# Performance work log

Hardware: AMD Instinct MI355X
Metric: run time of the kernel (lower is better)

The kernel has to match this reference:

```python
import jax, jax.numpy as jnp
import numpy as np

D_MODEL = 1024
N_HEAD = 16
D_K = 64
D_V = 64
D_INNER = 4096
MAX_REL = 16
EPS = 1e-6


def _rel_index(length_q, length_k):
    # Shaw-style clipped relative distance matrix -> indices into embedding table
    dist = jnp.arange(length_k)[None, :] - jnp.arange(length_q)[:, None]
    return jnp.clip(dist, -MAX_REL, MAX_REL) + MAX_REL  # [Lq, Lk] in [0, 2*MAX_REL]


def _layer_norm(x, gamma, beta):
    mu = jnp.mean(x, axis=-1, keepdims=True)
    var = jnp.var(x, axis=-1, keepdims=True)
    return (x - mu) / jnp.sqrt(var + EPS) * gamma + beta


def setup_inputs() -> dict:
    key = jax.random.key(0)
    ks = jax.random.split(key, 16)
    B, L = 8, 1024
    s = 0.02
    inp = {
        "q": jax.random.normal(ks[0], (B, L, D_MODEL), jnp.float32),
        "k": jax.random.normal(ks[1], (B, L, D_MODEL), jnp.float32),
        "v": jax.random.normal(ks[2], (B, L, D_MODEL), jnp.float32),
        "wq": jax.random.normal(ks[3], (D_MODEL, D_MODEL), jnp.float32) * s,
        "bq": jnp.zeros((D_MODEL,), jnp.float32),
        "wk": jax.random.normal(ks[4], (D_MODEL, D_MODEL), jnp.float32) * s,
        "bk": jnp.zeros((D_MODEL,), jnp.float32),
        "wv": jax.random.normal(ks[5], (D_MODEL, D_MODEL), jnp.float32) * s,
        "bv": jnp.zeros((D_MODEL,), jnp.float32),
        "wfc": jax.random.normal(ks[6], (D_MODEL, D_MODEL), jnp.float32) * s,
        "bfc": jnp.zeros((D_MODEL,), jnp.float32),
        "w1": jax.random.normal(ks[7], (D_MODEL, D_INNER), jnp.float32) * s,
        "b1": jnp.zeros((D_INNER,), jnp.float32),
        "w2": jax.random.normal(ks[8], (D_INNER, D_MODEL), jnp.float32) * s,
        "b2": jnp.zeros((D_MODEL,), jnp.float32),
        "ln_g": jnp.ones((D_MODEL,), jnp.float32),
        "ln_b": jnp.zeros((D_MODEL,), jnp.float32),
        "rel_k": jax.random.normal(ks[9], (2 * MAX_REL + 1, D_K), jnp.float32) * s,
        "rel_v": jax.random.normal(ks[10], (2 * MAX_REL + 1, D_V), jnp.float32) * s,
    }
    return inp


def reference(q, k, v, wq, bq, wk, bk, wv, bv, wfc, bfc, w1, b1, w2, b2, ln_g, ln_b, rel_k, rel_v):
    B, Lq, _ = q.shape
    Lk = k.shape[1]
    residual = q

    Q = q @ wq + bq  # [B, Lq, D]
    K = k @ wk + bk
    V = v @ wv + bv

    Qh = Q.reshape(B, Lq, N_HEAD, D_K)  # [B, Lq, H, dk]
    Kh = K.reshape(B, Lk, N_HEAD, D_K)
    Vh = V.reshape(B, Lk, N_HEAD, D_V)

    # content-content scores
    attn1 = jnp.einsum("bqhd,bkhd->bhqk", Qh, Kh)
    # content-position scores (Shaw relative position)
    idx = _rel_index(Lq, Lk)  # [Lq, Lk]
    k2 = rel_k[idx]           # [Lq, Lk, dk]
    attn2 = jnp.einsum("bqhd,qkd->bhqk", Qh, k2)

    attn = (attn1 + attn2) / jnp.sqrt(jnp.float32(D_K))
    attn = jax.nn.softmax(attn, axis=-1)  # dropout = identity (eval)

    weight1 = jnp.einsum("bhqk,bkhd->bhqd", attn, Vh)
    v2 = rel_v[idx]  # [Lq, Lk, dv]
    weight2 = jnp.einsum("bhqk,qkd->bhqd", attn, v2)

    out = (weight1 + weight2).transpose(0, 2, 1, 3).reshape(B, Lq, N_HEAD * D_V)
    out = out @ wfc + bfc
    out = out + residual
    out = _layer_norm(out, ln_g, ln_b)

    residual = out
    out2 = jax.nn.relu(out @ w1 + b1) @ w2 + b2
    out = _layer_norm(out2 + residual, ln_g, ln_b)  # same LN params reused, as in source
    return out
```

## Files before the change

kernel.cpp:

```cpp
#include <hip/hip_runtime.h>
#include <stdint.h>


typedef __bf16 bf16x8 __attribute__((ext_vector_type(8)));
typedef float  f32x4  __attribute__((ext_vector_type(4)));

__device__ __forceinline__ unsigned short f2bf(float f) {
  __bf16 h = (__bf16)f;
  union { __bf16 h; unsigned short u; } x; x.h = h;
  return x.u;
}
__device__ __forceinline__ float bf2f(unsigned short h) {
  union { unsigned u; float f; } x; x.u = ((unsigned)h) << 16; return x.f;
}

__device__ __forceinline__ void gload_lds16(
    const unsigned short* g,
    __attribute__((address_space(3))) unsigned int* l) {
  __builtin_amdgcn_global_load_lds(
      (const __attribute__((address_space(1))) unsigned int*)g, l, 16, 0, 0);
}

template<int EPI>
__global__ __launch_bounds__(256) void gemm_bt(
    const unsigned short* __restrict__ A,
    const unsigned short* __restrict__ Bt,
    const float* __restrict__ bias,
    void* __restrict__ Cout,
    int M, int N, int K)
{
  __shared__ __align__(16) unsigned short As[128 * 32];
  __shared__ __align__(16) unsigned short Bs[128 * 32];
  const int tid = threadIdx.x;
  const int lane = tid & 63, wv = tid >> 6;
  const int lq = lane >> 4, lm = lane & 15;
  const int wr = wv >> 1, wc = wv & 1;

  const int nx = gridDim.x;
  const int nwg = nx * gridDim.y;
  int bid = blockIdx.y * nx + blockIdx.x;
  bid = (bid & 7) * (nwg >> 3) + (bid >> 3);
  const int m0 = (bid / nx) * 128, n0 = (bid % nx) * 128;

  const unsigned short* ga0 = A  + (size_t)(m0 + (tid >> 2)) * K + (tid & 3) * 8;
  const unsigned short* gb0 = Bt + (size_t)(n0 + (tid >> 2)) * K + (tid & 3) * 8;
  const size_t rstep = (size_t)64 * K;

  __attribute__((address_space(3))) unsigned int* lA =
      (__attribute__((address_space(3))) unsigned int*)As + wv * 256;
  __attribute__((address_space(3))) unsigned int* lB =
      (__attribute__((address_space(3))) unsigned int*)Bs + wv * 256;

  const char* fa = (const char*)As + (wr * 64 + lm) * 64 + lq * 16;
  const char* fb = (const char*)Bs + (wc * 64 + lm) * 64 + lq * 16;

  f32x4 acc[4][4] = {};
  const int nk = K >> 5;
  for (int kt = 0; kt < nk; ++kt) {
    __syncthreads();
    gload_lds16(ga0,         lA);
    gload_lds16(ga0 + rstep, lA + 1024);
    gload_lds16(gb0,         lB);
    gload_lds16(gb0 + rstep, lB + 1024);
    ga0 += 32; gb0 += 32;
    __syncthreads();
    bf16x8 af[4], bfr[4];
    #pragma unroll
    for (int i = 0; i < 4; ++i) af[i]  = *(const bf16x8*)(fa + i * 16 * 64);
    #pragma unroll
    for (int j = 0; j < 4; ++j) bfr[j] = *(const bf16x8*)(fb + j * 16 * 64);
    #pragma unroll
    for (int i = 0; i < 4; ++i)
      #pragma unroll
      for (int j = 0; j < 4; ++j)
        acc[i][j] = __builtin_amdgcn_mfma_f32_16x16x32_bf16(af[i], bfr[j], acc[i][j], 0, 0, 0);
  }
  #pragma unroll
  for (int i = 0; i < 4; ++i) {
    #pragma unroll
    for (int j = 0; j < 4; ++j) {
      const int col = n0 + wc * 64 + j * 16 + lm;
      const float bv = bias[col];
      #pragma unroll
      for (int r = 0; r < 4; ++r) {
        const int row = m0 + wr * 64 + i * 16 + lq * 4 + r;
        float v = acc[i][j][r] + bv;
        if (EPI == 2) v = fmaxf(v, 0.0f);
        if (EPI == 1) ((float*)Cout)[(size_t)row * N + col] = v;
        else ((unsigned short*)Cout)[(size_t)row * N + col] = f2bf(v);
      }
    }
  }
}

__global__ __launch_bounds__(256) void tcast(
    const float* __restrict__ in, unsigned short* __restrict__ out, int R, int C)
{
  __shared__ float tile[32][33];
  const int tx = threadIdx.x & 31, ty = threadIdx.x >> 5;
  const int r0 = blockIdx.y * 32, c0 = blockIdx.x * 32;
  #pragma unroll
  for (int s = 0; s < 4; ++s)
    tile[ty + s * 8][tx] = in[(size_t)(r0 + ty + s * 8) * C + c0 + tx];
  __syncthreads();
  #pragma unroll
  for (int s = 0; s < 4; ++s)
    out[(size_t)(c0 + ty + s * 8) * R + r0 + tx] = f2bf(tile[tx][ty + s * 8]);
}

__global__ __launch_bounds__(256) void cast4(
    const float* __restrict__ in, unsigned short* __restrict__ out, int n)
{
  int i = (blockIdx.x * 256 + threadIdx.x) * 4;
  if (i < n) {
    float4 v = *(const float4*)(in + i);
    ushort4 o;
    o.x = f2bf(v.x); o.y = f2bf(v.y); o.z = f2bf(v.z); o.w = f2bf(v.w);
    *(ushort4*)(out + i) = o;
  }
}

__global__ __launch_bounds__(256) void vtrans(
    const unsigned short* __restrict__ VP, unsigned short* __restrict__ VPT)
{
  __shared__ unsigned short tile[64 * 66];
  const int pt = blockIdx.x, h = blockIdx.y, b = blockIdx.z;
  const int tid = threadIdx.x;
  const int p = tid >> 2, c0 = (tid & 3) * 16;
  const unsigned short* src = VP + (size_t)(b * 1024 + pt * 64 + p) * 1024 + h * 64 + c0;
  union { uint4 q; unsigned int u[4]; } t0, t1;
  t0.q = *(const uint4*)src;
  t1.q = *(const uint4*)(src + 8);
  #pragma unroll
  for (int e = 0; e < 4; ++e) {
    *(unsigned int*)&tile[p * 66 + c0 + e * 2]     = t0.u[e];
    *(unsigned int*)&tile[p * 66 + c0 + 8 + e * 2] = t1.u[e];
  }
  __syncthreads();
  const int d = tid >> 2, p0 = (tid & 3) * 16;
  union { uint4 q[2]; unsigned short s[16]; } ob;
  #pragma unroll
  for (int e = 0; e < 16; ++e) ob.s[e] = tile[(p0 + e) * 66 + d];
  unsigned short* dst = VPT + ((size_t)(h * 64 + d) * 8 + b) * 1024 + pt * 64 + p0;
  *(uint4*)dst       = ob.q[0];
  *(uint4*)(dst + 8) = ob.q[1];
}

__global__ __launch_bounds__(256, 3) void attn_flash(
    const unsigned short* __restrict__ Qp,
    const unsigned short* __restrict__ Kp,
    const unsigned short* __restrict__ VPT,
    const float* __restrict__ relk,
    const float* __restrict__ relv,
    unsigned short* __restrict__ ctx)
{
  const int qt = blockIdx.x, h = blockIdx.y, b = blockIdx.z;
  const int tid = threadIdx.x;
  const int lane = tid & 63, wv = tid >> 6;
  const int lq = lane >> 4, lm = lane & 15;

  __shared__ __align__(16) unsigned short Kt[64][72];
  __shared__ __align__(16) unsigned short Vt[64][72];
  __shared__ __align__(16) unsigned short Pt[64][72];
  __shared__ __align__(16) unsigned short relvT[64][32];
  __shared__ float qrel_s[64][33];
  __shared__ float Racc[64][33];

  const float CE = 0.125f * 1.44269504088896340736f;

  const int tok0 = b * 1024 + qt * 64;

  for (int i = tid; i < 64 * 33; i += 256) {
    const int rr = i / 33, ss = i - rr * 33;
    Racc[rr][ss] = 0.0f;
  }
  for (int i = tid; i < 64 * 32; i += 256) {
    const int dd = i >> 5, ss = i & 31;
    relvT[dd][ss] = f2bf(relv[ss * 64 + dd]);
  }

  bf16x8 qf0, qf1;
  {
    const unsigned short* qg = Qp + (size_t)(tok0 + wv * 16 + lm) * 1024 + h * 64;
    qf0 = *(const bf16x8*)(qg + lq * 8);
    qf1 = *(const bf16x8*)(qg + 32 + lq * 8);
  }

  #pragma unroll
  for (int t = 0; t < 3; ++t) {
    const int bin = t * 16 + lm;
    union { bf16x8 v; unsigned short s[8]; } rk0, rk1;
    #pragma unroll
    for (int e = 0; e < 8; ++e) { rk0.s[e] = 0; rk1.s[e] = 0; }
    if (bin < 33) {
      const float* rp = relk + bin * 64 + lq * 8;
      #pragma unroll
      for (int e = 0; e < 8; ++e) {
        rk0.s[e] = f2bf(rp[e]);
        rk1.s[e] = f2bf(rp[32 + e]);
      }
    }
    f32x4 Sr = {};
    Sr = __builtin_amdgcn_mfma_f32_16x16x32_bf16(qf0, rk0.v, Sr, 0, 0, 0);
    Sr = __builtin_amdgcn_mfma_f32_16x16x32_bf16(qf1, rk1.v, Sr, 0, 0, 0);
    if (bin < 33) {
      #pragma unroll
      for (int r = 0; r < 4; ++r) qrel_s[wv * 16 + lq * 4 + r][bin] = Sr[r] * CE;
    }
  }
  __syncthreads();

  float q0a[4], q32a[4];
  #pragma unroll
  for (int r = 0; r < 4; ++r) {
    const int rowl = wv * 16 + lq * 4 + r;
    q0a[r]  = qrel_s[rowl][0];
    q32a[r] = qrel_s[rowl][32];
  }

  union { bf16x8 v; unsigned short s[8]; } one8;
  #pragma unroll
  for (int e = 0; e < 8; ++e) one8.s[e] = 0x3F80;

  f32x4 Oa[4] = {};
  f32x4 Rs = {};
  float r0a[4] = {0, 0, 0, 0}, r32a[4] = {0, 0, 0, 0};

  const int srow = tid >> 2, scol = (tid & 3) * 16;
  const unsigned short* kg = Kp + (size_t)(b * 1024 + srow) * 1024 + h * 64 + scol;
  const unsigned short* vg = VPT + ((size_t)(h * 64 + srow) * 8 + b) * 1024 + scol;
  const int qa0 = qt * 64 + wv * 16;

  for (int kt = 0; kt < 16; ++kt) {
    __syncthreads();
    *(uint4*)&Kt[srow][scol]     = *(const uint4*)(kg);
    *(uint4*)&Kt[srow][scol + 8] = *(const uint4*)(kg + 8);
    *(uint4*)&Vt[srow][scol]     = *(const uint4*)(vg);
    *(uint4*)&Vt[srow][scol + 8] = *(const uint4*)(vg + 8);
    kg += 64 * 1024;
    vg += 64;
    __syncthreads();

    #pragma unroll
    for (int tj = 0; tj < 4; ++tj) {
      bf16x8 kf0 = *(const bf16x8*)(&Kt[tj * 16 + lm][lq * 8]);
      bf16x8 kf1 = *(const bf16x8*)(&Kt[tj * 16 + lm][32 + lq * 8]);
      f32x4 S = {};
      S = __builtin_amdgcn_mfma_f32_16x16x32_bf16(qf0, kf0, S, 0, 0, 0);
      S = __builtin_amdgcn_mfma_f32_16x16x32_bf16(qf1, kf1, S, 0, 0, 0);
      const int c0 = kt * 64 + tj * 16;
      if (c0 + 31 <= qa0) {
        #pragma unroll
        for (int r = 0; r < 4; ++r) {
          const float p = __builtin_amdgcn_exp2f(fmaf(S[r], CE, q0a[r]));
          r0a[r] += p;
          Pt[wv * 16 + lq * 4 + r][tj * 16 + lm] = f2bf(p);
        }
      } else if (c0 >= qa0 + 31) {
        #pragma unroll
        for (int r = 0; r < 4; ++r) {
          const float p = __builtin_amdgcn_exp2f(fmaf(S[r], CE, q32a[r]));
          r32a[r] += p;
          Pt[wv * 16 + lq * 4 + r][tj * 16 + lm] = f2bf(p);
        }
      } else {
        const int kpos = c0 + lm;
        #pragma unroll
        for (int r = 0; r < 4; ++r) {
          const int rowl = wv * 16 + lq * 4 + r;
          const int dist = kpos - (qt * 64 + rowl);
          const int bin = (dist < -16 ? 0 : (dist > 16 ? 32 : dist + 16));
          const float p = __builtin_amdgcn_exp2f(fmaf(S[r], CE, qrel_s[rowl][bin]));
          if (bin == 0)       r0a[r]  += p;
          else if (bin == 32) r32a[r] += p;
          else Racc[rowl][bin] = p;
          Pt[rowl][tj * 16 + lm] = f2bf(p);
        }
      }
    }
    __syncthreads();
    const int prow = wv * 16 + lm;
    bf16x8 pf0 = *(const bf16x8*)(&Pt[prow][lq * 8]);
    bf16x8 pf1 = *(const bf16x8*)(&Pt[prow][32 + lq * 8]);
    Rs = __builtin_amdgcn_mfma_f32_16x16x32_bf16(pf0, one8.v, Rs, 0, 0, 0);
    Rs = __builtin_amdgcn_mfma_f32_16x16x32_bf16(pf1, one8.v, Rs, 0, 0, 0);
    #pragma unroll
    for (int dt = 0; dt < 4; ++dt) {
      bf16x8 vf0 = *(const bf16x8*)(&Vt[dt * 16 + lm][lq * 8]);
      bf16x8 vf1 = *(const bf16x8*)(&Vt[dt * 16 + lm][32 + lq * 8]);
      Oa[dt] = __builtin_amdgcn_mfma_f32_16x16x32_bf16(pf0, vf0, Oa[dt], 0, 0, 0);
      Oa[dt] = __builtin_amdgcn_mfma_f32_16x16x32_bf16(pf1, vf1, Oa[dt], 0, 0, 0);
    }
  }

  #pragma unroll
  for (int r = 0; r < 4; ++r) {
    #pragma unroll
    for (int off = 1; off < 16; off <<= 1) {
      r0a[r]  += __shfl_xor(r0a[r],  off, 64);
      r32a[r] += __shfl_xor(r32a[r], off, 64);
    }
  }
  if (lm == 0) {
    #pragma unroll
    for (int r = 0; r < 4; ++r) Racc[wv * 16 + lq * 4 + r][0] = r0a[r];
  }
  __syncthreads();
  for (int i = tid; i < 64 * 32; i += 256) {
    const int rr = i >> 5, cc = i & 31;
    Pt[rr][cc] = f2bf(Racc[rr][cc]);
  }
  __syncthreads();

  bf16x8 raf = *(const bf16x8*)(&Pt[wv * 16 + lm][lq * 8]);
  #pragma unroll
  for (int dt = 0; dt < 4; ++dt) {
    bf16x8 rvb = *(const bf16x8*)(&relvT[dt * 16 + lm][lq * 8]);
    f32x4 O2 = {};
    O2 = __builtin_amdgcn_mfma_f32_16x16x32_bf16(raf, rvb, O2, 0, 0, 0);
    const float rv32 = relv[32 * 64 + dt * 16 + lm];
    #pragma unroll
    for (int r = 0; r < 4; ++r) {
      const int rowl = wv * 16 + lq * 4 + r;
      const float v = (Oa[dt][r] + O2[r] + r32a[r] * rv32) / Rs[r];
      ctx[(size_t)(tok0 + rowl) * 1024 + h * 64 + dt * 16 + lm] = f2bf(v);
    }
  }
}

template<bool WB>
__global__ __launch_bounds__(256) void ln_res(
    const float* __restrict__ x, const float* __restrict__ res,
    const float* __restrict__ g, const float* __restrict__ bta,
    float* __restrict__ of, unsigned short* __restrict__ ob)
{
  const int row = blockIdx.x;
  const int tid = threadIdx.x;
  __shared__ float red[8];
  const size_t base = (size_t)row * 1024 + tid * 4;
  const float4 xv = *(const float4*)(x + base);
  const float4 rv = *(const float4*)(res + base);
  float v0 = xv.x + rv.x, v1 = xv.y + rv.y, v2 = xv.z + rv.z, v3 = xv.w + rv.w;
  float s1 = v0 + v1 + v2 + v3;
  float s2 = v0 * v0 + v1 * v1 + v2 * v2 + v3 * v3;
  #pragma unroll
  for (int off = 1; off < 64; off <<= 1) {
    s1 += __shfl_xor(s1, off, 64);
    s2 += __shfl_xor(s2, off, 64);
  }
  const int wv = tid >> 6;
  if ((tid & 63) == 0) { red[wv * 2] = s1; red[wv * 2 + 1] = s2; }
  __syncthreads();
  s1 = red[0] + red[2] + red[4] + red[6];
  s2 = red[1] + red[3] + red[5] + red[7];
  const float mean = s1 * (1.f / 1024.f);
  const float var = s2 * (1.f / 1024.f) - mean * mean;
  const float rstd = rsqrtf(var + 1e-6f);
  const float4 gv = *(const float4*)(g + tid * 4);
  const float4 bv = *(const float4*)(bta + tid * 4);
  float y0 = (v0 - mean) * rstd * gv.x + bv.x;
  float y1 = (v1 - mean) * rstd * gv.y + bv.y;
  float y2 = (v2 - mean) * rstd * gv.z + bv.z;
  float y3 = (v3 - mean) * rstd * gv.w + bv.w;
  float4 yo; yo.x = y0; yo.y = y1; yo.z = y2; yo.w = y3;
  *(float4*)(of + base) = yo;
  if (WB) {
    ushort4 o;
    o.x = f2bf(y0); o.y = f2bf(y1); o.z = f2bf(y2); o.w = f2bf(y3);
    *(ushort4*)(ob + base) = o;
  }
}

extern "C" void kernel_launch(void* const* d_in, const int* in_sizes, int n_in,
                              void* d_out, int out_size, void* d_ws, size_t ws_size,
                              hipStream_t stream) {
  (void)in_sizes; (void)n_in; (void)out_size; (void)ws_size;
  const float* q    = (const float*)d_in[0];
  const float* k    = (const float*)d_in[1];
  const float* v    = (const float*)d_in[2];
  const float* wq   = (const float*)d_in[3];
  const float* bq   = (const float*)d_in[4];
  const float* wk   = (const float*)d_in[5];
  const float* bk   = (const float*)d_in[6];
  const float* wv_  = (const float*)d_in[7];
  const float* bv   = (const float*)d_in[8];
  const float* wfc  = (const float*)d_in[9];
  const float* bfc  = (const float*)d_in[10];
  const float* w1   = (const float*)d_in[11];
  const float* b1   = (const float*)d_in[12];
  const float* w2   = (const float*)d_in[13];
  const float* b2   = (const float*)d_in[14];
  const float* ln_g = (const float*)d_in[15];
  const float* ln_b = (const float*)d_in[16];
  const float* rel_k = (const float*)d_in[17];
  const float* rel_v = (const float*)d_in[18];

  char* ws = (char*)d_ws;
  const size_t MB = 1ull << 20;
  unsigned short* WQT  = (unsigned short*)(ws + 0 * MB);
  unsigned short* WKT  = (unsigned short*)(ws + 2 * MB);
  unsigned short* WVT  = (unsigned short*)(ws + 4 * MB);
  unsigned short* WFCT = (unsigned short*)(ws + 6 * MB);
  unsigned short* W1T  = (unsigned short*)(ws + 8 * MB);
  unsigned short* W2T  = (unsigned short*)(ws + 16 * MB);
  unsigned short* QP   = (unsigned short*)(ws + 24 * MB);
  unsigned short* KP   = (unsigned short*)(ws + 40 * MB);
  unsigned short* VP   = (unsigned short*)(ws + 56 * MB);
  unsigned short* QBF  = (unsigned short*)(ws + 72 * MB);
  unsigned short* KBF  = (unsigned short*)(ws + 88 * MB);
  unsigned short* VBF  = (unsigned short*)(ws + 104 * MB);
  unsigned short* VPT  = QBF;
  unsigned short* CTX  = KBF;
  float*          OTMP = (float*)(ws + 104 * MB);
  float*          X1F  = (float*)(ws + 24 * MB);
  unsigned short* X1BF = VP;
  unsigned short* HBUF = (unsigned short*)(ws + 72 * MB);
  float*          Y2   = (float*)(ws + 136 * MB);

  const dim3 blk(256);
  const int NTOK = 8192;

  tcast<<<dim3(32, 32), blk, 0, stream>>>(wq, WQT, 1024, 1024);
  tcast<<<dim3(32, 32), blk, 0, stream>>>(wk, WKT, 1024, 1024);
  tcast<<<dim3(32, 32), blk, 0, stream>>>(wv_, WVT, 1024, 1024);
  tcast<<<dim3(32, 32), blk, 0, stream>>>(wfc, WFCT, 1024, 1024);
  tcast<<<dim3(128, 32), blk, 0, stream>>>(w1, W1T, 1024, 4096);
  tcast<<<dim3(32, 128), blk, 0, stream>>>(w2, W2T, 4096, 1024);
  cast4<<<8192, blk, 0, stream>>>(q, QBF, NTOK * 1024);
  cast4<<<8192, blk, 0, stream>>>(k, KBF, NTOK * 1024);
  cast4<<<8192, blk, 0, stream>>>(v, VBF, NTOK * 1024);

  gemm_bt<0><<<dim3(8, 64), blk, 0, stream>>>(QBF, WQT, bq, QP, NTOK, 1024, 1024);
  gemm_bt<0><<<dim3(8, 64), blk, 0, stream>>>(KBF, WKT, bk, KP, NTOK, 1024, 1024);
  gemm_bt<0><<<dim3(8, 64), blk, 0, stream>>>(VBF, WVT, bv, VP, NTOK, 1024, 1024);

  vtrans<<<dim3(16, 16, 8), blk, 0, stream>>>(VP, VPT);

  attn_flash<<<dim3(16, 16, 8), blk, 0, stream>>>(QP, KP, VPT, rel_k, rel_v, CTX);

  gemm_bt<1><<<dim3(8, 64), blk, 0, stream>>>(CTX, WFCT, bfc, OTMP, NTOK, 1024, 1024);
  ln_res<true><<<8192, blk, 0, stream>>>(OTMP, q, ln_g, ln_b, X1F, X1BF);
  gemm_bt<2><<<dim3(32, 64), blk, 0, stream>>>(X1BF, W1T, b1, HBUF, NTOK, 4096, 1024);
  gemm_bt<1><<<dim3(8, 64), blk, 0, stream>>>(HBUF, W2T, b2, Y2, NTOK, 1024, 4096);
  ln_res<false><<<8192, blk, 0, stream>>>(Y2, X1F, ln_g, ln_b, (float*)d_out, nullptr);
}
```

Before: 659.8 us.

## Prefetch K/V tiles into registers, swizzle block order, remap P-tile row layout

```diff
diff --git a/kernel.cpp b/kernel.cpp
--- a/kernel.cpp
+++ b/kernel.cpp
@@ -154,7 +154,10 @@
     const float* __restrict__ relv,
     unsigned short* __restrict__ ctx)
 {
-  const int qt = blockIdx.x, h = blockIdx.y, b = blockIdx.z;
+  int id = (blockIdx.z * gridDim.y + blockIdx.y) * gridDim.x + blockIdx.x;
+  id = (id & 7) * 256 + (id >> 3);
+  const int qt = id & 15, h = (id >> 4) & 15, b = id >> 8;
+
   const int tid = threadIdx.x;
   const int lane = tid & 63, wv = tid >> 6;
   const int lq = lane >> 4, lm = lane & 15;
@@ -231,14 +234,27 @@
   const unsigned short* vg = VPT + ((size_t)(h * 64 + srow) * 8 + b) * 1024 + scol;
   const int qa0 = qt * 64 + wv * 16;
 
+  const int pread = wv * 16 + ((lm & 3) << 2) + (lm >> 2);
+
+  uint4 rk0_ = *(const uint4*)(kg);
+  uint4 rk1_ = *(const uint4*)(kg + 8);
+  uint4 rv0_ = *(const uint4*)(vg);
+  uint4 rv1_ = *(const uint4*)(vg + 8);
+
   for (int kt = 0; kt < 16; ++kt) {
     __syncthreads();
-    *(uint4*)&Kt[srow][scol]     = *(const uint4*)(kg);
-    *(uint4*)&Kt[srow][scol + 8] = *(const uint4*)(kg + 8);
-    *(uint4*)&Vt[srow][scol]     = *(const uint4*)(vg);
-    *(uint4*)&Vt[srow][scol + 8] = *(const uint4*)(vg + 8);
-    kg += 64 * 1024;
-    vg += 64;
+    *(uint4*)&Kt[srow][scol]     = rk0_;
+    *(uint4*)&Kt[srow][scol + 8] = rk1_;
+    *(uint4*)&Vt[srow][scol]     = rv0_;
+    *(uint4*)&Vt[srow][scol + 8] = rv1_;
+    if (kt < 15) {
+      kg += 64 * 1024;
+      vg += 64;
+      rk0_ = *(const uint4*)(kg);
+      rk1_ = *(const uint4*)(kg + 8);
+      rv0_ = *(const uint4*)(vg);
+      rv1_ = *(const uint4*)(vg + 8);
+    }
     __syncthreads();
 
     #pragma unroll
@@ -249,19 +265,20 @@
       S = __builtin_amdgcn_mfma_f32_16x16x32_bf16(qf0, kf0, S, 0, 0, 0);
       S = __builtin_amdgcn_mfma_f32_16x16x32_bf16(qf1, kf1, S, 0, 0, 0);
       const int c0 = kt * 64 + tj * 16;
+      const int prow0 = wv * 16 + lq;
       if (c0 + 31 <= qa0) {
         #pragma unroll
         for (int r = 0; r < 4; ++r) {
           const float p = __builtin_amdgcn_exp2f(fmaf(S[r], CE, q0a[r]));
           r0a[r] += p;
-          Pt[wv * 16 + lq * 4 + r][tj * 16 + lm] = f2bf(p);
+          Pt[prow0 + r * 4][tj * 16 + lm] = f2bf(p);
         }
       } else if (c0 >= qa0 + 31) {
         #pragma unroll
         for (int r = 0; r < 4; ++r) {
           const float p = __builtin_amdgcn_exp2f(fmaf(S[r], CE, q32a[r]));
           r32a[r] += p;
-          Pt[wv * 16 + lq * 4 + r][tj * 16 + lm] = f2bf(p);
+          Pt[prow0 + r * 4][tj * 16 + lm] = f2bf(p);
         }
       } else {
         const int kpos = c0 + lm;
@@ -274,14 +291,13 @@
           if (bin == 0)       r0a[r]  += p;
           else if (bin == 32) r32a[r] += p;
           else Racc[rowl][bin] = p;
-          Pt[rowl][tj * 16 + lm] = f2bf(p);
+          Pt[prow0 + r * 4][tj * 16 + lm] = f2bf(p);
         }
       }
     }
     __syncthreads();
-    const int prow = wv * 16 + lm;
-    bf16x8 pf0 = *(const bf16x8*)(&Pt[prow][lq * 8]);
-    bf16x8 pf1 = *(const bf16x8*)(&Pt[prow][32 + lq * 8]);
+    bf16x8 pf0 = *(const bf16x8*)(&Pt[pread][lq * 8]);
+    bf16x8 pf1 = *(const bf16x8*)(&Pt[pread][32 + lq * 8]);
     Rs = __builtin_amdgcn_mfma_f32_16x16x32_bf16(pf0, one8.v, Rs, 0, 0, 0);
     Rs = __builtin_amdgcn_mfma_f32_16x16x32_bf16(pf1, one8.v, Rs, 0, 0, 0);
     #pragma unroll
```

Measured after the change: 647.2 us. About the same (-1.9%).
